# Kernel tuning notes

Hardware: AMD Instinct MI355X
Metric: run time of the kernel (lower is better)

Reference implementation:

```python
import jax, jax.numpy as jnp
import numpy as np

NB_X = 32
NB_Y = 32
EPS = 1e-08


def setup_inputs() -> dict:
    key = jax.random.key(0)
    ks = jax.random.split(key, 10)
    B, L, F, H, D = 16, NB_X * NB_Y + 1, 768, 12, 64
    s = 0.02
    return {
        'x': jax.random.normal(ks[0], (B, L, F), dtype=jnp.float32),
        'wq': jax.random.normal(ks[1], (F, H, D), dtype=jnp.float32) * s,
        'bq': jnp.zeros((H, D), dtype=jnp.float32),
        'wk': jax.random.normal(ks[2], (F, H, D), dtype=jnp.float32) * s,
        'bk': jnp.zeros((H, D), dtype=jnp.float32),
        'wv': jax.random.normal(ks[3], (F, H, D), dtype=jnp.float32) * s,
        'bv': jnp.zeros((H, D), dtype=jnp.float32),
        'wo': jax.random.normal(ks[4], (H, D, F), dtype=jnp.float32) * s,
        'bo': jnp.zeros((F,), dtype=jnp.float32),
        'toeplitz_params': jax.random.normal(ks[5], (H, 4 * NB_X * NB_Y), dtype=jnp.float32),
    }


def _dist_index():
    # relative-position index over the 2D patch grid, flattened to (L0*L0,)
    gi = np.arange(NB_X)
    gj = np.arange(NB_Y)
    idx = ((gi[:, None, None, None] - gi[None, None, :, None] + NB_X) * 2 * NB_Y
           + gj[None, :, None, None] - gj[None, None, None, :] + NB_Y)
    return jnp.asarray(idx.reshape(-1), dtype=jnp.int32)


def reference(x, wq, bq, wk, bk, wv, bv, wo, bo, toeplitz_params):
    H, D = wq.shape[1], wq.shape[2]
    L0 = NB_X * NB_Y  # number of patch tokens (seq len = L0 + 1 with CLS)

    q = jnp.einsum('bqf,fhd->bqhd', x, wq) + bq
    k = jnp.einsum('bkf,fhd->bkhd', x, wk) + bk
    v = jnp.einsum('bkf,fhd->bkhd', x, wv) + bv

    # relu-kernelized scores
    q = jax.nn.relu(q / jnp.sqrt(jnp.float32(D))) + EPS
    k = jax.nn.relu(k) + EPS
    attn = jnp.einsum('bqhd,bkhd->bhqk', q, k)  # [B,H,L,L]

    # per-head Toeplitz relative-position mask via gather
    tm = jnp.take(toeplitz_params, _dist_index(), axis=1).reshape(H, L0, L0)
    tm = jnp.pad(tm, [[0, 0], [1, 0], [0, 0]], constant_values=1.0)
    tm = jnp.pad(tm, [[0, 0], [0, 0], [1, 0]], constant_values=1.0)

    attn = attn * jnp.abs(tm)[None] + EPS
    attn = attn / jnp.sum(attn, axis=-1, keepdims=True)  # sum-normalization

    out = jnp.einsum('bhqk,bkhd->bqhd', attn, v)
    return jnp.einsum('bqhd,hdf->bqf', out, wo) + bo
```

## Files before the change

### kernel.cpp

```cpp
#include <hip/hip_runtime.h>
#include <hip/hip_bf16.h>

#define BB 16
#define LQ 1025
#define FF 768
#define HH 12
#define DD 64
#define EPSF 1e-8f

#define TPSTRIDE 6400
#define QPART_CLS 6270
#define VSTRIDE 1040

#define LDK 72

typedef unsigned short u16;
typedef __attribute__((ext_vector_type(8))) short  bf16x8;
typedef __attribute__((ext_vector_type(4))) float  f32x4;

__device__ __forceinline__ float bf2f(u16 u) {
    union { unsigned int i; float f; } c;
    c.i = ((unsigned int)u) << 16;
    return c.f;
}

__device__ __forceinline__ u16 f2bf(float f) {
    union { float f; unsigned int i; } c;
    c.f = f;
    unsigned int x = c.i;
    unsigned int r = (x + 0x7fffu + ((x >> 16) & 1u)) >> 16;
    return (u16)r;
}

__global__ __launch_bounds__(256) void convert_x(
    const float* __restrict__ x, u16* __restrict__ xb, int n4)
{
    int i = blockIdx.x * blockDim.x + threadIdx.x;
    const int stride = gridDim.x * blockDim.x;
    for (; i < n4; i += stride) {
        float4 f = ((const float4*)x)[i];
        ushort4 o;
        o.x = f2bf(f.x); o.y = f2bf(f.y); o.z = f2bf(f.z); o.w = f2bf(f.w);
        ((ushort4*)xb)[i] = o;
    }
}

__global__ __launch_bounds__(256) void transpose_w(
    const float* __restrict__ wq, const float* __restrict__ wk,
    const float* __restrict__ wv, const float* __restrict__ wo,
    u16* __restrict__ wqt, u16* __restrict__ wkt,
    u16* __restrict__ wvt, u16* __restrict__ wot)
{
    const int z = blockIdx.z;
    const float* __restrict__ src = (z == 0) ? wq : (z == 1) ? wk : (z == 2) ? wv : wo;
    u16* __restrict__ dst         = (z == 0) ? wqt : (z == 1) ? wkt : (z == 2) ? wvt : wot;

    const int c0 = blockIdx.x * 64;
    const int r0 = blockIdx.y * 64;

    __shared__ u16 tile[64][72];

    const int t   = threadIdx.x;
    const int row = t >> 2;
    const int cs  = (t & 3) << 4;

    {
        const float* p = src + (size_t)(r0 + row) * 768 + c0 + cs;
#pragma unroll
        for (int q = 0; q < 4; ++q) {
            float4 f = *(const float4*)(p + 4 * q);
            ushort4 o;
            o.x = f2bf(f.x); o.y = f2bf(f.y); o.z = f2bf(f.z); o.w = f2bf(f.w);
            *(ushort4*)&tile[row][cs + 4 * q] = o;
        }
    }
    __syncthreads();
    {
        u16* p = dst + (size_t)(c0 + row) * 768 + r0 + cs;
#pragma unroll
        for (int q = 0; q < 4; ++q) {
            ushort4 o;
            o.x = tile[cs + 4 * q + 0][row];
            o.y = tile[cs + 4 * q + 1][row];
            o.z = tile[cs + 4 * q + 2][row];
            o.w = tile[cs + 4 * q + 3][row];
            *(ushort4*)(p + 4 * q) = o;
        }
    }
}

__global__ __launch_bounds__(256) void build_tpa(
    const float* __restrict__ tp, float* __restrict__ tpa)
{
    int i = blockIdx.x * 256 + threadIdx.x;
    if (i >= HH * TPSTRIDE) return;
    int h = i / TPSTRIDE, j = i - h * TPSTRIDE;
    float v;
    if (j < 64) v = 0.f;
    else if (j < 64 + 4096) v = fabsf(tp[h * 4096 + (j - 64)]);
    else v = 1.f;
    tpa[i] = v;
}

__global__ __launch_bounds__(256) void pack_bias(
    const float* __restrict__ bq, const float* __restrict__ bk,
    const float* __restrict__ bv, float* __restrict__ bias_cat)
{
    int i = blockIdx.x * 256 + threadIdx.x;
    if (i >= 2304) return;
    float v = (i < 768) ? bq[i] : (i < 1536) ? bk[i - 768] : bv[i - 1536];
    bias_cat[i] = v;
}

__global__ __launch_bounds__(256) void transpose_v(
    const u16* __restrict__ vbuf, u16* __restrict__ vtbuf)
{
    const int bh = blockIdx.y;
    const int lt = blockIdx.x;
    __shared__ u16 tile[64][65];
    const int t   = threadIdx.x;
    const int row = t >> 2;
    const int seg = (t & 3) << 4;

    {
        int l = lt * 64 + row;
        if (l < LQ) {
            const ushort4* p = (const ushort4*)(vbuf + ((size_t)bh * LQ + l) * 64 + seg);
#pragma unroll
            for (int q = 0; q < 4; ++q) {
                ushort4 a = p[q];
                tile[row][seg + 4 * q + 0] = a.x;
                tile[row][seg + 4 * q + 1] = a.y;
                tile[row][seg + 4 * q + 2] = a.z;
                tile[row][seg + 4 * q + 3] = a.w;
            }
        } else {
#pragma unroll
            for (int j = 0; j < 16; ++j) tile[row][seg + j] = 0;
        }
    }
    __syncthreads();
    {
        int kbase = lt * 64 + seg;
        if (kbase + 16 <= VSTRIDE) {
            u16* q = vtbuf + (size_t)bh * 64 * VSTRIDE + (size_t)row * VSTRIDE + kbase;
#pragma unroll
            for (int g = 0; g < 4; ++g) {
                ushort4 o;
                o.x = tile[seg + 4 * g + 0][row];
                o.y = tile[seg + 4 * g + 1][row];
                o.z = tile[seg + 4 * g + 2][row];
                o.w = tile[seg + 4 * g + 3][row];
                *(ushort4*)(q + 4 * g) = o;
            }
        }
    }
}

__global__ __launch_bounds__(256) void gemm_qkv_mfma(
    const u16* __restrict__ xb, const u16* __restrict__ wt,
    const float* __restrict__ bias_cat,
    u16* __restrict__ qbuf, u16* __restrict__ kbuf, u16* __restrict__ vbuf)
{
    const int M   = BB * LQ;
    const int m0  = blockIdx.x * 128;
    const int n0g = blockIdx.y * 128;

    __shared__ u16 As[128 * LDK];
    __shared__ u16 Bs[128 * LDK];

    const int t    = threadIdx.x;
    const int wave = t >> 6;
    const int lane = t & 63;
    const int quad = lane >> 4;
    const int l16  = lane & 15;
    const int wm   = (wave >> 1) << 6;
    const int wn   = (wave & 1) << 6;

    const int sm   = t >> 1;
    const int sc   = (t & 1) << 5;

    const bool avalid = (m0 + sm) < M;
    const u16* pa = xb + (size_t)(m0 + sm) * 768 + sc;
    const u16* pb = wt + (size_t)(n0g + sm) * 768 + sc;

    f32x4 acc[4][4];
#pragma unroll
    for (int i = 0; i < 4; ++i)
#pragma unroll
        for (int j = 0; j < 4; ++j)
            acc[i][j] = (f32x4){0.f, 0.f, 0.f, 0.f};

    for (int k0 = 0; k0 < 768; k0 += 64) {
        __syncthreads();
        if (avalid) {
            const uint4* p = (const uint4*)(pa + k0);
#pragma unroll
            for (int q = 0; q < 4; ++q)
                *(uint4*)&As[sm * LDK + sc + 8 * q] = p[q];
        } else {
            uint4 z; z.x = 0; z.y = 0; z.z = 0; z.w = 0;
#pragma unroll
            for (int q = 0; q < 4; ++q)
                *(uint4*)&As[sm * LDK + sc + 8 * q] = z;
        }
        {
            const uint4* p = (const uint4*)(pb + k0);
#pragma unroll
            for (int q = 0; q < 4; ++q)
                *(uint4*)&Bs[sm * LDK + sc + 8 * q] = p[q];
        }
        __syncthreads();

#pragma unroll
        for (int h2 = 0; h2 < 2; ++h2) {
            bf16x8 af[4], bf[4];
#pragma unroll
            for (int i = 0; i < 4; ++i)
                af[i] = *(const bf16x8*)&As[(wm + 16 * i + l16) * LDK + h2 * 32 + quad * 8];
#pragma unroll
            for (int j = 0; j < 4; ++j)
                bf[j] = *(const bf16x8*)&Bs[(wn + 16 * j + l16) * LDK + h2 * 32 + quad * 8];
#pragma unroll
            for (int i = 0; i < 4; ++i)
#pragma unroll
                for (int j = 0; j < 4; ++j)
                    acc[i][j] = __builtin_amdgcn_mfma_f32_16x16x32_bf16(af[i], bf[j], acc[i][j], 0, 0, 0);
        }
    }

    const int type = (n0g >= 1536) ? 2 : (n0g >= 768) ? 1 : 0;
    u16* __restrict__ outb = (type == 0) ? qbuf : (type == 1) ? kbuf : vbuf;
    const int nbase = n0g - type * 768;

#pragma unroll
    for (int i = 0; i < 4; ++i) {
#pragma unroll
        for (int reg = 0; reg < 4; ++reg) {
            int gm = m0 + wm + 16 * i + quad * 4 + reg;
            if (gm >= M) continue;
            int b_idx = gm / LQ;
            int l     = gm - b_idx * LQ;
#pragma unroll
            for (int j = 0; j < 4; ++j) {
                int nloc = nbase + wn + 16 * j + l16;
                int h = nloc >> 6, d = nloc & 63;
                float v = acc[i][j][reg] + bias_cat[n0g + wn + 16 * j + l16];
                if (type == 0) v = fmaxf(v * 0.125f, 0.f) + EPSF;
                else if (type == 1) v = fmaxf(v, 0.f) + EPSF;
                outb[((size_t)(b_idx * HH + h) * LQ + l) * 64 + d] = f2bf(v);
            }
        }
    }
}

__global__ __launch_bounds__(256) void attn_fused(
    const u16* __restrict__ qbuf, const u16* __restrict__ kbuf,
    const u16* __restrict__ vtbuf, const float* __restrict__ tpa,
    u16* __restrict__ obuf)
{
    const int bh = blockIdx.y;
    const int b  = bh / HH;
    const int h  = bh - b * HH;
    const int q0 = blockIdx.x * 64;

    __shared__ u16 SQ[64][72];
    __shared__ u16 Ks[2][64][72];
    __shared__ u16 Vt[2][64][72];

    const int t    = threadIdx.x;
    const int wave = t >> 6;
    const int lane = t & 63;
    const int quad = lane >> 4;
    const int l16  = lane & 15;
    const int w16  = wave << 4;

    const size_t base  = (size_t)bh * LQ * 64;
    const size_t vbase = (size_t)bh * 64 * VSTRIDE;
    const float* tb = tpa + h * TPSTRIDE;

    const int srow = t >> 2;
    const int sseg = (t & 3) << 4;

    {
        const uint4* qp = (const uint4*)(qbuf + base + (size_t)(q0 + srow) * 64 + sseg);
        *(uint4*)&SQ[srow][sseg]     = qp[0];
        *(uint4*)&SQ[srow][sseg + 8] = qp[1];
    }

    const int qi = q0 + w16 + l16;
    int qpart;
    if (qi == 0) qpart = QPART_CLS;
    else { int qm1 = qi - 1; qpart = (((qm1 >> 5) + 32) << 6) + (qm1 & 31) + 32; }

    int idx[16];
#pragma unroll
    for (int ct = 0; ct < 4; ++ct)
#pragma unroll
        for (int reg = 0; reg < 4; ++reg) {
            int km1 = ct * 16 + quad * 4 + reg - 1;
            idx[ct * 4 + reg] = 64 + qpart - (((km1 >> 5) << 6) + (km1 & 31));
        }

    uint4 kr0, kr1, vr0, vr1;
    {
        uint4 z; z.x = 0; z.y = 0; z.z = 0; z.w = 0;
        int ki = srow;
        if (ki < LQ) {
            const uint4* kp = (const uint4*)(kbuf + base + (size_t)ki * 64 + sseg);
            kr0 = kp[0]; kr1 = kp[1];
        } else { kr0 = z; kr1 = z; }
        const uint4* vp = (const uint4*)(vtbuf + vbase + (size_t)srow * VSTRIDE + sseg);
        vr0 = vp[0]; vr1 = vp[1];
    }

    __syncthreads();

    bf16x8 qf0 = *(const bf16x8*)&SQ[w16 + l16][quad * 8];
    bf16x8 qf1 = *(const bf16x8*)&SQ[w16 + l16][32 + quad * 8];

    *(uint4*)&Ks[0][srow][sseg]     = kr0;
    *(uint4*)&Ks[0][srow][sseg + 8] = kr1;
    *(uint4*)&Vt[0][srow][sseg]     = vr0;
    *(uint4*)&Vt[0][srow][sseg + 8] = vr1;

    {
        uint4 z; z.x = 0; z.y = 0; z.z = 0; z.w = 0;
        int ki = 64 + srow;
        if (ki < LQ) {
            const uint4* kp = (const uint4*)(kbuf + base + (size_t)ki * 64 + sseg);
            kr0 = kp[0]; kr1 = kp[1];
        } else { kr0 = z; kr1 = z; }
        int vcol = 64 + sseg;
        const uint4* vp = (const uint4*)(vtbuf + vbase + (size_t)srow * VSTRIDE + vcol);
        vr0 = vp[0]; vr1 = vp[1];
    }

    f32x4 acc_o[4];
#pragma unroll
    for (int dt = 0; dt < 4; ++dt) acc_o[dt] = (f32x4){0.f, 0.f, 0.f, 0.f};
    float den = 0.f;

    __syncthreads();

    for (int kt = 0; kt < 17; ++kt) {
        const int p = kt & 1;

        if (kt < 16) {
            *(uint4*)&Ks[p ^ 1][srow][sseg]     = kr0;
            *(uint4*)&Ks[p ^ 1][srow][sseg + 8] = kr1;
            *(uint4*)&Vt[p ^ 1][srow][sseg]     = vr0;
            *(uint4*)&Vt[p ^ 1][srow][sseg + 8] = vr1;
        }
        if (kt < 15) {
            uint4 z; z.x = 0; z.y = 0; z.z = 0; z.w = 0;
            int k0n = (kt + 2) * 64;
            int ki = k0n + srow;
            if (ki < LQ) {
                const uint4* kp = (const uint4*)(kbuf + base + (size_t)ki * 64 + sseg);
                kr0 = kp[0]; kr1 = kp[1];
            } else { kr0 = z; kr1 = z; }
            int vcol = k0n + sseg;
            if (vcol + 16 <= VSTRIDE) {
                const uint4* vp = (const uint4*)(vtbuf + vbase + (size_t)srow * VSTRIDE + vcol);
                vr0 = vp[0]; vr1 = vp[1];
            } else { vr0 = z; vr1 = z; }
        }

        float tmv[16];
#pragma unroll
        for (int e = 0; e < 16; ++e) tmv[e] = tb[idx[e]];

        f32x4 acc_s[4];
#pragma unroll
        for (int ct = 0; ct < 4; ++ct) {
            bf16x8 kf0 = *(const bf16x8*)&Ks[p][ct * 16 + l16][quad * 8];
            bf16x8 kf1 = *(const bf16x8*)&Ks[p][ct * 16 + l16][32 + quad * 8];
            f32x4 z = (f32x4){0.f, 0.f, 0.f, 0.f};
            z = __builtin_amdgcn_mfma_f32_16x16x32_bf16(kf0, qf0, z, 0, 0, 0);
            z = __builtin_amdgcn_mfma_f32_16x16x32_bf16(kf1, qf1, z, 0, 0, 0);
            acc_s[ct] = z;
        }

        if (kt == 0) { if (quad == 0) tmv[0] = 1.0f; }

#pragma unroll
        for (int ct = 0; ct < 4; ++ct) {
            float s0 = acc_s[ct][0] * tmv[ct * 4 + 0] + EPSF;
            float s1 = acc_s[ct][1] * tmv[ct * 4 + 1] + EPSF;
            float s2 = acc_s[ct][2] * tmv[ct * 4 + 2] + EPSF;
            float s3 = acc_s[ct][3] * tmv[ct * 4 + 3] + EPSF;
            den += (s0 + s1) + (s2 + s3);
            ushort4 w;
            w.x = f2bf(s0); w.y = f2bf(s1); w.z = f2bf(s2); w.w = f2bf(s3);
            *(ushort4*)&SQ[w16 + l16][ct * 16 + quad * 4] = w;
        }
#pragma unroll
        for (int e = 0; e < 16; ++e) idx[e] -= 128;

        {
            bf16x8 a0 = *(const bf16x8*)&SQ[w16 + l16][quad * 8];
            bf16x8 a1 = *(const bf16x8*)&SQ[w16 + l16][32 + quad * 8];
#pragma unroll
            for (int dt = 0; dt < 4; ++dt) {
                bf16x8 b0 = *(const bf16x8*)&Vt[p][dt * 16 + l16][quad * 8];
                bf16x8 b1 = *(const bf16x8*)&Vt[p][dt * 16 + l16][32 + quad * 8];
                acc_o[dt] = __builtin_amdgcn_mfma_f32_16x16x32_bf16(a0, b0, acc_o[dt], 0, 0, 0);
                acc_o[dt] = __builtin_amdgcn_mfma_f32_16x16x32_bf16(a1, b1, acc_o[dt], 0, 0, 0);
            }
        }

        if (kt < 16) __syncthreads();
    }

    den += __shfl_xor(den, 16);
    den += __shfl_xor(den, 32);
    float invd = 1.f / den;

#pragma unroll
    for (int reg = 0; reg < 4; ++reg) {
        int r = quad * 4 + reg;
        float iv = __shfl(invd, r, 64);
        int qrow = q0 + w16 + r;
        if (qrow < LQ) {
            u16* p = obuf + ((size_t)(b * LQ + qrow) * HH + h) * 64;
#pragma unroll
            for (int dt = 0; dt < 4; ++dt)
                p[dt * 16 + l16] = f2bf(acc_o[dt][reg] * iv);
        }
    }
}

__global__ __launch_bounds__(256) void gemm_out_mfma(
    const u16* __restrict__ a, const u16* __restrict__ wot,
    const float* __restrict__ bo, float* __restrict__ out)
{
    const int M  = BB * LQ;
    const int m0 = blockIdx.x * 128;
    const int n0 = blockIdx.y * 128;

    __shared__ u16 As[128 * LDK];
    __shared__ u16 Bs[128 * LDK];

    const int t    = threadIdx.x;
    const int wave = t >> 6;
    const int lane = t & 63;
    const int quad = lane >> 4;
    const int l16  = lane & 15;
    const int wm   = (wave >> 1) << 6;
    const int wn   = (wave & 1) << 6;

    const int sm   = t >> 1;
    const int sc   = (t & 1) << 5;

    const bool avalid = (m0 + sm) < M;
    const u16* pa = a   + (size_t)(m0 + sm) * 768 + sc;
    const u16* pb = wot + (size_t)(n0 + sm) * 768 + sc;

    f32x4 acc[4][4];
#pragma unroll
    for (int i = 0; i < 4; ++i)
#pragma unroll
        for (int j = 0; j < 4; ++j)
            acc[i][j] = (f32x4){0.f, 0.f, 0.f, 0.f};

    for (int k0 = 0; k0 < 768; k0 += 64) {
        __syncthreads();
        if (avalid) {
            const uint4* p = (const uint4*)(pa + k0);
#pragma unroll
            for (int q = 0; q < 4; ++q)
                *(uint4*)&As[sm * LDK + sc + 8 * q] = p[q];
        } else {
            uint4 z; z.x = 0; z.y = 0; z.z = 0; z.w = 0;
#pragma unroll
            for (int q = 0; q < 4; ++q)
                *(uint4*)&As[sm * LDK + sc + 8 * q] = z;
        }
        {
            const uint4* p = (const uint4*)(pb + k0);
#pragma unroll
            for (int q = 0; q < 4; ++q)
                *(uint4*)&Bs[sm * LDK + sc + 8 * q] = p[q];
        }
        __syncthreads();

#pragma unroll
        for (int h2 = 0; h2 < 2; ++h2) {
            bf16x8 af[4], bf[4];
#pragma unroll
            for (int i = 0; i < 4; ++i)
                af[i] = *(const bf16x8*)&As[(wm + 16 * i + l16) * LDK + h2 * 32 + quad * 8];
#pragma unroll
            for (int j = 0; j < 4; ++j)
                bf[j] = *(const bf16x8*)&Bs[(wn + 16 * j + l16) * LDK + h2 * 32 + quad * 8];
#pragma unroll
            for (int i = 0; i < 4; ++i)
#pragma unroll
                for (int j = 0; j < 4; ++j)
                    acc[i][j] = __builtin_amdgcn_mfma_f32_16x16x32_bf16(af[i], bf[j], acc[i][j], 0, 0, 0);
        }
    }

#pragma unroll
    for (int i = 0; i < 4; ++i) {
#pragma unroll
        for (int reg = 0; reg < 4; ++reg) {
            int gm = m0 + wm + 16 * i + quad * 4 + reg;
            if (gm >= M) continue;
            float* p = out + (size_t)gm * 768;
#pragma unroll
            for (int j = 0; j < 4; ++j) {
                int n = n0 + wn + 16 * j + l16;
                p[n] = acc[i][j][reg] + bo[n];
            }
        }
    }
}

extern "C" void kernel_launch(void* const* d_in, const int* in_sizes, int n_in,
                              void* d_out, int out_size, void* d_ws, size_t ws_size,
                              hipStream_t stream) {
    const float* x  = (const float*)d_in[0];
    const float* wq = (const float*)d_in[1];
    const float* bq = (const float*)d_in[2];
    const float* wk = (const float*)d_in[3];
    const float* bk = (const float*)d_in[4];
    const float* wv = (const float*)d_in[5];
    const float* bv = (const float*)d_in[6];
    const float* wo = (const float*)d_in[7];
    const float* bo = (const float*)d_in[8];
    const float* tp = (const float*)d_in[9];
    float* out = (float*)d_out;

    const size_t per = (size_t)BB * HH * LQ * DD;
    const size_t wsz = (size_t)FF * FF;
    u16* ws16  = (u16*)d_ws;
    u16* qbuf  = ws16;
    u16* kbuf  = qbuf + per;
    u16* vbuf  = kbuf + per;
    u16* xb    = vbuf + per;
    u16* wqt   = xb + per;
    u16* wkt   = wqt + wsz;
    u16* wvt   = wkt + wsz;
    u16* wot   = wvt + wsz;
    float* tpa = (float*)(wot + wsz);
    float* bias_cat = tpa + HH * TPSTRIDE;

    u16* vtbuf = xb;
    u16* obuf  = vbuf;

    convert_x<<<2048, 256, 0, stream>>>(x, xb, (int)(per / 4));
    dim3 gt(12, 12, 4);
    transpose_w<<<gt, 256, 0, stream>>>(wq, wk, wv, wo, wqt, wkt, wvt, wot);
    build_tpa<<<(HH * TPSTRIDE + 255) / 256, 256, 0, stream>>>(tp, tpa);
    pack_bias<<<9, 256, 0, stream>>>(bq, bk, bv, bias_cat);

    dim3 g1(129, 18);
    gemm_qkv_mfma<<<g1, 256, 0, stream>>>(xb, wqt, bias_cat, qbuf, kbuf, vbuf);

    dim3 gv(17, BB * HH);
    transpose_v<<<gv, 256, 0, stream>>>(vbuf, vtbuf);

    dim3 g2(17, BB * HH);
    attn_fused<<<g2, 256, 0, stream>>>(qbuf, kbuf, vtbuf, tpa, obuf);

    dim3 g3(129, 6);
    gemm_out_mfma<<<g3, 256, 0, stream>>>(obuf, wot, bo, out);
}
```

Before: 455.5 us.

## Precompute dense per-head Toeplitz mask and stream it in attention

Adds a kernel that expands the abs Toeplitz parameters into a dense padded [H,1088,1088] fp32 mask in workspace. A new attention kernel then reads each mask row as float4 vectors instead of doing gathered index arithmetic per score. The cost is an extra ~57MB write per call plus heavier global traffic from the dense mask, which should stay largely L2/MALL-resident across batches. The new path only runs when the workspace is large enough.

```diff
diff --git a/kernel.cpp b/kernel.cpp
--- a/kernel.cpp
+++ b/kernel.cpp
@@ -11,6 +11,7 @@
 #define TPSTRIDE 6400
 #define QPART_CLS 6270
 #define VSTRIDE 1040
+#define TMQ 1088
 
 #define LDK 72
 
@@ -102,6 +103,30 @@
     tpa[i] = v;
 }
 
+__global__ __launch_bounds__(256) void build_tmfull(
+    const float* __restrict__ tpa, float* __restrict__ tmf)
+{
+    const int h  = blockIdx.y;
+    const int qi = blockIdx.x;
+    const float* tb = tpa + h * TPSTRIDE;
+    float* row = tmf + ((size_t)h * TMQ + qi) * TMQ;
+
+    int qpart;
+    if (qi == 0) qpart = QPART_CLS;
+    else { int qm1 = qi - 1; qpart = (((qm1 >> 5) + 32) << 6) + (qm1 & 31) + 32; }
+
+    for (int kg = threadIdx.x; kg < TMQ; kg += 256) {
+        float v;
+        if (kg == 0) v = 1.0f;
+        else {
+            int km1 = kg - 1;
+            int kpart = ((km1 >> 5) << 6) + (km1 & 31);
+            v = tb[64 + qpart - kpart];
+        }
+        row[kg] = v;
+    }
+}
+
 __global__ __launch_bounds__(256) void pack_bias(
     const float* __restrict__ bq, const float* __restrict__ bk,
     const float* __restrict__ bv, float* __restrict__ bias_cat)
@@ -250,6 +275,169 @@
                 else if (type == 1) v = fmaxf(v, 0.f) + EPSF;
                 outb[((size_t)(b_idx * HH + h) * LQ + l) * 64 + d] = f2bf(v);
             }
+        }
+    }
+}
+
+__global__ __launch_bounds__(256) void attn_fused_tm(
+    const u16* __restrict__ qbuf, const u16* __restrict__ kbuf,
+    const u16* __restrict__ vtbuf, const float* __restrict__ tmf,
+    u16* __restrict__ obuf)
+{
+    const int bh = blockIdx.y;
+    const int b  = bh / HH;
+    const int h  = bh - b * HH;
+    const int q0 = blockIdx.x * 64;
+
+    __shared__ u16 SQ[64][72];
+    __shared__ u16 Ks[2][64][72];
+    __shared__ u16 Vt[2][64][72];
+
+    const int t    = threadIdx.x;
+    const int wave = t >> 6;
+    const int lane = t & 63;
+    const int quad = lane >> 4;
+    const int l16  = lane & 15;
+    const int w16  = wave << 4;
+
+    const size_t base  = (size_t)bh * LQ * 64;
+    const size_t vbase = (size_t)bh * 64 * VSTRIDE;
+
+    const int srow = t >> 2;
+    const int sseg = (t & 3) << 4;
+
+    {
+        const uint4* qp = (const uint4*)(qbuf + base + (size_t)(q0 + srow) * 64 + sseg);
+        *(uint4*)&SQ[srow][sseg]     = qp[0];
+        *(uint4*)&SQ[srow][sseg + 8] = qp[1];
+    }
+
+    const int qi = q0 + w16 + l16;
+    const float* tml = tmf + ((size_t)h * TMQ + qi) * TMQ + quad * 4;
+
+    uint4 kr0, kr1, vr0, vr1;
+    {
+        uint4 z; z.x = 0; z.y = 0; z.z = 0; z.w = 0;
+        int ki = srow;
+        if (ki < LQ) {
+            const uint4* kp = (const uint4*)(kbuf + base + (size_t)ki * 64 + sseg);
+            kr0 = kp[0]; kr1 = kp[1];
+        } else { kr0 = z; kr1 = z; }
+        const uint4* vp = (const uint4*)(vtbuf + vbase + (size_t)srow * VSTRIDE + sseg);
+        vr0 = vp[0]; vr1 = vp[1];
+    }
+
+    __syncthreads();
+
+    bf16x8 qf0 = *(const bf16x8*)&SQ[w16 + l16][quad * 8];
+    bf16x8 qf1 = *(const bf16x8*)&SQ[w16 + l16][32 + quad * 8];
+
+    *(uint4*)&Ks[0][srow][sseg]     = kr0;
+    *(uint4*)&Ks[0][srow][sseg + 8] = kr1;
+    *(uint4*)&Vt[0][srow][sseg]     = vr0;
+    *(uint4*)&Vt[0][srow][sseg + 8] = vr1;
+
+    {
+        uint4 z; z.x = 0; z.y = 0; z.z = 0; z.w = 0;
+        int ki = 64 + srow;
+        if (ki < LQ) {
+            const uint4* kp = (const uint4*)(kbuf + base + (size_t)ki * 64 + sseg);
+            kr0 = kp[0]; kr1 = kp[1];
+        } else { kr0 = z; kr1 = z; }
+        int vcol = 64 + sseg;
+        const uint4* vp = (const uint4*)(vtbuf + vbase + (size_t)srow * VSTRIDE + vcol);
+        vr0 = vp[0]; vr1 = vp[1];
+    }
+
+    f32x4 acc_o[4];
+#pragma unroll
+    for (int dt = 0; dt < 4; ++dt) acc_o[dt] = (f32x4){0.f, 0.f, 0.f, 0.f};
+    float den = 0.f;
+
+    __syncthreads();
+
+    for (int kt = 0; kt < 17; ++kt) {
+        const int p = kt & 1;
+
+        if (kt < 16) {
+            *(uint4*)&Ks[p ^ 1][srow][sseg]     = kr0;
+            *(uint4*)&Ks[p ^ 1][srow][sseg + 8] = kr1;
+            *(uint4*)&Vt[p ^ 1][srow][sseg]     = vr0;
+            *(uint4*)&Vt[p ^ 1][srow][sseg + 8] = vr1;
+        }
+        if (kt < 15) {
+            uint4 z; z.x = 0; z.y = 0; z.z = 0; z.w = 0;
+            int k0n = (kt + 2) * 64;
+            int ki = k0n + srow;
+            if (ki < LQ) {
+                const uint4* kp = (const uint4*)(kbuf + base + (size_t)ki * 64 + sseg);
+                kr0 = kp[0]; kr1 = kp[1];
+            } else { kr0 = z; kr1 = z; }
+            int vcol = k0n + sseg;
+            if (vcol + 16 <= VSTRIDE) {
+                const uint4* vp = (const uint4*)(vtbuf + vbase + (size_t)srow * VSTRIDE + vcol);
+                vr0 = vp[0]; vr1 = vp[1];
+            } else { vr0 = z; vr1 = z; }
+        }
+
+        float4 tm4[4];
+#pragma unroll
+        for (int ct = 0; ct < 4; ++ct)
+            tm4[ct] = *(const float4*)(tml + ct * 16);
+
+        f32x4 acc_s[4];
+#pragma unroll
+        for (int ct = 0; ct < 4; ++ct) {
+            bf16x8 kf0 = *(const bf16x8*)&Ks[p][ct * 16 + l16][quad * 8];
+            bf16x8 kf1 = *(const bf16x8*)&Ks[p][ct * 16 + l16][32 + quad * 8];
+            f32x4 z = (f32x4){0.f, 0.f, 0.f, 0.f};
+            z = __builtin_amdgcn_mfma_f32_16x16x32_bf16(kf0, qf0, z, 0, 0, 0);
+            z = __builtin_amdgcn_mfma_f32_16x16x32_bf16(kf1, qf1, z, 0, 0, 0);
+            acc_s[ct] = z;
+        }
+
+#pragma unroll
+        for (int ct = 0; ct < 4; ++ct) {
+            float s0 = acc_s[ct][0] * tm4[ct].x + EPSF;
+            float s1 = acc_s[ct][1] * tm4[ct].y + EPSF;
+            float s2 = acc_s[ct][2] * tm4[ct].z + EPSF;
+            float s3 = acc_s[ct][3] * tm4[ct].w + EPSF;
+            den += (s0 + s1) + (s2 + s3);
+            ushort4 w;
+            w.x = f2bf(s0); w.y = f2bf(s1); w.z = f2bf(s2); w.w = f2bf(s3);
+            *(ushort4*)&SQ[w16 + l16][ct * 16 + quad * 4] = w;
+        }
+        tml += 64;
+
+        {
+            bf16x8 a0 = *(const bf16x8*)&SQ[w16 + l16][quad * 8];
+            bf16x8 a1 = *(const bf16x8*)&SQ[w16 + l16][32 + quad * 8];
+#pragma unroll
+            for (int dt = 0; dt < 4; ++dt) {
+                bf16x8 b0 = *(const bf16x8*)&Vt[p][dt * 16 + l16][quad * 8];
+                bf16x8 b1 = *(const bf16x8*)&Vt[p][dt * 16 + l16][32 + quad * 8];
+                acc_o[dt] = __builtin_amdgcn_mfma_f32_16x16x32_bf16(a0, b0, acc_o[dt], 0, 0, 0);
+                acc_o[dt] = __builtin_amdgcn_mfma_f32_16x16x32_bf16(a1, b1, acc_o[dt], 0, 0, 0);
+            }
+        }
+
+        if (kt < 16) __syncthreads();
+    }
+
+    den += __shfl_xor(den, 16);
+    den += __shfl_xor(den, 32);
+    float invd = 1.f / den;
+
+#pragma unroll
+    for (int reg = 0; reg < 4; ++reg) {
+        int r = quad * 4 + reg;
+        float iv = __shfl(invd, r, 64);
+        int qrow = q0 + w16 + r;
+        if (qrow < LQ) {
+            u16* p = obuf + ((size_t)(b * LQ + qrow) * HH + h) * 64;
+#pragma unroll
+            for (int dt = 0; dt < 4; ++dt)
+                p[dt * 16 + l16] = f2bf(acc_o[dt][reg] * iv);
         }
     }
 }
@@ -546,15 +734,24 @@
     u16* wot   = wvt + wsz;
     float* tpa = (float*)(wot + wsz);
     float* bias_cat = tpa + HH * TPSTRIDE;
+    float* tmfull   = bias_cat + 2304;
 
     u16* vtbuf = xb;
     u16* obuf  = vbuf;
+
+    const size_t tm_off = (size_t)((char*)tmfull - (char*)d_ws);
+    const size_t tm_bytes = (size_t)HH * TMQ * TMQ * sizeof(float);
+    const bool use_tm = ws_size >= tm_off + tm_bytes;
 
     convert_x<<<2048, 256, 0, stream>>>(x, xb, (int)(per / 4));
     dim3 gt(12, 12, 4);
     transpose_w<<<gt, 256, 0, stream>>>(wq, wk, wv, wo, wqt, wkt, wvt, wot);
     build_tpa<<<(HH * TPSTRIDE + 255) / 256, 256, 0, stream>>>(tp, tpa);
     pack_bias<<<9, 256, 0, stream>>>(bq, bk, bv, bias_cat);
+    if (use_tm) {
+        dim3 gm(TMQ, HH);
+        build_tmfull<<<gm, 256, 0, stream>>>(tpa, tmfull);
+    }
 
     dim3 g1(129, 18);
     gemm_qkv_mfma<<<g1, 256, 0, stream>>>(xb, wqt, bias_cat, qbuf, kbuf, vbuf);
@@ -563,7 +760,10 @@
     transpose_v<<<gv, 256, 0, stream>>>(vbuf, vtbuf);
 
     dim3 g2(17, BB * HH);
-    attn_fused<<<g2, 256, 0, stream>>>(qbuf, kbuf, vtbuf, tpa, obuf);
+    if (use_tm)
+        attn_fused_tm<<<g2, 256, 0, stream>>>(qbuf, kbuf, vtbuf, tmfull, obuf);
+    else
+        attn_fused<<<g2, 256, 0, stream>>>(qbuf, kbuf, vtbuf, tpa, obuf);
 
     dim3 g3(129, 6);
     gemm_out_mfma<<<g3, 256, 0, stream>>>(obuf, wot, bo, out);
```

Measured after the change: 518.7 us. 1.14x slower.

## Read K/V fragments directly from global memory in attention, dropping LDS staging

Applied to the files above, without the earlier changes.

The attention kernel no longer stages K and V tiles through double-buffered shared memory. Each wave now loads its MFMA fragments straight from global memory, and the per-tile __syncthreads barriers are removed. To drop the bounds checks, the K buffer is padded to 1088 rows with a new kernel that zeroes the tail, and the transposed-V stride is widened to match. The aim is to cut LDS traffic and barrier stalls. In exchange, every wave re-reads the same K/V through the caches, and with the loop left un-unrolled there is no explicit prefetch to hide global load latency.

```diff
diff --git a/kernel.cpp b/kernel.cpp
--- a/kernel.cpp
+++ b/kernel.cpp
@@ -10,7 +10,8 @@
 
 #define TPSTRIDE 6400
 #define QPART_CLS 6270
-#define VSTRIDE 1040
+#define VSTRIDE 1088
+#define KPAD 1088
 
 #define LDK 72
 
@@ -112,6 +113,19 @@
     bias_cat[i] = v;
 }
 
+__global__ __launch_bounds__(256) void zero_ktail(u16* __restrict__ kbuf)
+{
+    int i = blockIdx.x * 256 + threadIdx.x;
+    const int N = BB * HH * (KPAD - LQ) * 16;
+    if (i >= N) return;
+    int bh  = i / ((KPAD - LQ) * 16);
+    int r   = i - bh * ((KPAD - LQ) * 16);
+    int row = LQ + (r >> 4);
+    int seg = (r & 15) << 2;
+    ushort4 z; z.x = 0; z.y = 0; z.z = 0; z.w = 0;
+    *(ushort4*)(kbuf + ((size_t)bh * KPAD + row) * 64 + seg) = z;
+}
+
 __global__ __launch_bounds__(256) void transpose_v(
     const u16* __restrict__ vbuf, u16* __restrict__ vtbuf)
 {
@@ -232,6 +246,7 @@
     const int type = (n0g >= 1536) ? 2 : (n0g >= 768) ? 1 : 0;
     u16* __restrict__ outb = (type == 0) ? qbuf : (type == 1) ? kbuf : vbuf;
     const int nbase = n0g - type * 768;
+    const int lst   = (type == 1) ? KPAD : LQ;
 
 #pragma unroll
     for (int i = 0; i < 4; ++i) {
@@ -248,7 +263,7 @@
                 float v = acc[i][j][reg] + bias_cat[n0g + wn + 16 * j + l16];
                 if (type == 0) v = fmaxf(v * 0.125f, 0.f) + EPSF;
                 else if (type == 1) v = fmaxf(v, 0.f) + EPSF;
-                outb[((size_t)(b_idx * HH + h) * LQ + l) * 64 + d] = f2bf(v);
+                outb[((size_t)(b_idx * HH + h) * lst + l) * 64 + d] = f2bf(v);
             }
         }
     }
@@ -265,8 +280,6 @@
     const int q0 = blockIdx.x * 64;
 
     __shared__ u16 SQ[64][72];
-    __shared__ u16 Ks[2][64][72];
-    __shared__ u16 Vt[2][64][72];
 
     const int t    = threadIdx.x;
     const int wave = t >> 6;
@@ -275,20 +288,16 @@
     const int l16  = lane & 15;
     const int w16  = wave << 4;
 
-    const size_t base  = (size_t)bh * LQ * 64;
-    const size_t vbase = (size_t)bh * 64 * VSTRIDE;
+    const u16* qb = qbuf  + (size_t)bh * LQ * 64;
+    const u16* kb = kbuf  + (size_t)bh * KPAD * 64;
+    const u16* vb = vtbuf + (size_t)bh * 64 * VSTRIDE;
     const float* tb = tpa + h * TPSTRIDE;
 
-    const int srow = t >> 2;
-    const int sseg = (t & 3) << 4;
-
-    {
-        const uint4* qp = (const uint4*)(qbuf + base + (size_t)(q0 + srow) * 64 + sseg);
-        *(uint4*)&SQ[srow][sseg]     = qp[0];
-        *(uint4*)&SQ[srow][sseg + 8] = qp[1];
-    }
-
     const int qi = q0 + w16 + l16;
+    const u16* qp = qb + (size_t)qi * 64 + quad * 8;
+    bf16x8 qf0 = *(const bf16x8*)(qp);
+    bf16x8 qf1 = *(const bf16x8*)(qp + 32);
+
     int qpart;
     if (qi == 0) qpart = QPART_CLS;
     else { int qm1 = qi - 1; qpart = (((qm1 >> 5) + 32) << 6) + (qm1 & 31) + 32; }
@@ -302,71 +311,20 @@
             idx[ct * 4 + reg] = 64 + qpart - (((km1 >> 5) << 6) + (km1 & 31));
         }
 
-    uint4 kr0, kr1, vr0, vr1;
-    {
-        uint4 z; z.x = 0; z.y = 0; z.z = 0; z.w = 0;
-        int ki = srow;
-        if (ki < LQ) {
-            const uint4* kp = (const uint4*)(kbuf + base + (size_t)ki * 64 + sseg);
-            kr0 = kp[0]; kr1 = kp[1];
-        } else { kr0 = z; kr1 = z; }
-        const uint4* vp = (const uint4*)(vtbuf + vbase + (size_t)srow * VSTRIDE + sseg);
-        vr0 = vp[0]; vr1 = vp[1];
-    }
-
-    __syncthreads();
-
-    bf16x8 qf0 = *(const bf16x8*)&SQ[w16 + l16][quad * 8];
-    bf16x8 qf1 = *(const bf16x8*)&SQ[w16 + l16][32 + quad * 8];
-
-    *(uint4*)&Ks[0][srow][sseg]     = kr0;
-    *(uint4*)&Ks[0][srow][sseg + 8] = kr1;
-    *(uint4*)&Vt[0][srow][sseg]     = vr0;
-    *(uint4*)&Vt[0][srow][sseg + 8] = vr1;
-
-    {
-        uint4 z; z.x = 0; z.y = 0; z.z = 0; z.w = 0;
-        int ki = 64 + srow;
-        if (ki < LQ) {
-            const uint4* kp = (const uint4*)(kbuf + base + (size_t)ki * 64 + sseg);
-            kr0 = kp[0]; kr1 = kp[1];
-        } else { kr0 = z; kr1 = z; }
-        int vcol = 64 + sseg;
-        const uint4* vp = (const uint4*)(vtbuf + vbase + (size_t)srow * VSTRIDE + vcol);
-        vr0 = vp[0]; vr1 = vp[1];
-    }
+    const u16* kp  = kb + (size_t)l16 * 64 + quad * 8;
+    const u16* kp2 = kp + 2048;
+    const u16* vr0 = vb + (size_t)l16 * VSTRIDE + quad * 8;
+    const u16* vr1 = vr0 + 16 * VSTRIDE;
+    const u16* vr2 = vr0 + 32 * VSTRIDE;
+    const u16* vr3 = vr0 + 48 * VSTRIDE;
 
     f32x4 acc_o[4];
 #pragma unroll
     for (int dt = 0; dt < 4; ++dt) acc_o[dt] = (f32x4){0.f, 0.f, 0.f, 0.f};
     float den = 0.f;
 
-    __syncthreads();
-
+#pragma unroll 1
     for (int kt = 0; kt < 17; ++kt) {
-        const int p = kt & 1;
-
-        if (kt < 16) {
-            *(uint4*)&Ks[p ^ 1][srow][sseg]     = kr0;
-            *(uint4*)&Ks[p ^ 1][srow][sseg + 8] = kr1;
-            *(uint4*)&Vt[p ^ 1][srow][sseg]     = vr0;
-            *(uint4*)&Vt[p ^ 1][srow][sseg + 8] = vr1;
-        }
-        if (kt < 15) {
-            uint4 z; z.x = 0; z.y = 0; z.z = 0; z.w = 0;
-            int k0n = (kt + 2) * 64;
-            int ki = k0n + srow;
-            if (ki < LQ) {
-                const uint4* kp = (const uint4*)(kbuf + base + (size_t)ki * 64 + sseg);
-                kr0 = kp[0]; kr1 = kp[1];
-            } else { kr0 = z; kr1 = z; }
-            int vcol = k0n + sseg;
-            if (vcol + 16 <= VSTRIDE) {
-                const uint4* vp = (const uint4*)(vtbuf + vbase + (size_t)srow * VSTRIDE + vcol);
-                vr0 = vp[0]; vr1 = vp[1];
-            } else { vr0 = z; vr1 = z; }
-        }
-
         float tmv[16];
 #pragma unroll
         for (int e = 0; e < 16; ++e) tmv[e] = tb[idx[e]];
@@ -374,8 +332,9 @@
         f32x4 acc_s[4];
 #pragma unroll
         for (int ct = 0; ct < 4; ++ct) {
-            bf16x8 kf0 = *(const bf16x8*)&Ks[p][ct * 16 + l16][quad * 8];
-            bf16x8 kf1 = *(const bf16x8*)&Ks[p][ct * 16 + l16][32 + quad * 8];
+            const u16* kr = ((ct & 2) ? kp2 : kp) + (ct & 1) * 1024;
+            bf16x8 kf0 = *(const bf16x8*)(kr);
+            bf16x8 kf1 = *(const bf16x8*)(kr + 32);
             f32x4 z = (f32x4){0.f, 0.f, 0.f, 0.f};
             z = __builtin_amdgcn_mfma_f32_16x16x32_bf16(kf0, qf0, z, 0, 0, 0);
             z = __builtin_amdgcn_mfma_f32_16x16x32_bf16(kf1, qf1, z, 0, 0, 0);
@@ -401,16 +360,31 @@
         {
             bf16x8 a0 = *(const bf16x8*)&SQ[w16 + l16][quad * 8];
             bf16x8 a1 = *(const bf16x8*)&SQ[w16 + l16][32 + quad * 8];
-#pragma unroll
-            for (int dt = 0; dt < 4; ++dt) {
-                bf16x8 b0 = *(const bf16x8*)&Vt[p][dt * 16 + l16][quad * 8];
-                bf16x8 b1 = *(const bf16x8*)&Vt[p][dt * 16 + l16][32 + quad * 8];
-                acc_o[dt] = __builtin_amdgcn_mfma_f32_16x16x32_bf16(a0, b0, acc_o[dt], 0, 0, 0);
-                acc_o[dt] = __builtin_amdgcn_mfma_f32_16x16x32_bf16(a1, b1, acc_o[dt], 0, 0, 0);
-            }
-        }
-
-        if (kt < 16) __syncthreads();
+
+            bf16x8 b00 = *(const bf16x8*)(vr0);
+            bf16x8 b01 = *(const bf16x8*)(vr0 + 32);
+            acc_o[0] = __builtin_amdgcn_mfma_f32_16x16x32_bf16(a0, b00, acc_o[0], 0, 0, 0);
+            acc_o[0] = __builtin_amdgcn_mfma_f32_16x16x32_bf16(a1, b01, acc_o[0], 0, 0, 0);
+
+            bf16x8 b10 = *(const bf16x8*)(vr1);
+            bf16x8 b11 = *(const bf16x8*)(vr1 + 32);
+            acc_o[1] = __builtin_amdgcn_mfma_f32_16x16x32_bf16(a0, b10, acc_o[1], 0, 0, 0);
+            acc_o[1] = __builtin_amdgcn_mfma_f32_16x16x32_bf16(a1, b11, acc_o[1], 0, 0, 0);
+
+            bf16x8 b20 = *(const bf16x8*)(vr2);
+            bf16x8 b21 = *(const bf16x8*)(vr2 + 32);
+            acc_o[2] = __builtin_amdgcn_mfma_f32_16x16x32_bf16(a0, b20, acc_o[2], 0, 0, 0);
+            acc_o[2] = __builtin_amdgcn_mfma_f32_16x16x32_bf16(a1, b21, acc_o[2], 0, 0, 0);
+
+            bf16x8 b30 = *(const bf16x8*)(vr3);
+            bf16x8 b31 = *(const bf16x8*)(vr3 + 32);
+            acc_o[3] = __builtin_amdgcn_mfma_f32_16x16x32_bf16(a0, b30, acc_o[3], 0, 0, 0);
+            acc_o[3] = __builtin_amdgcn_mfma_f32_16x16x32_bf16(a1, b31, acc_o[3], 0, 0, 0);
+        }
+
+        kp  += 64 * 64;
+        kp2 += 64 * 64;
+        vr0 += 64; vr1 += 64; vr2 += 64; vr3 += 64;
     }
 
     den += __shfl_xor(den, 16);
@@ -533,12 +507,13 @@
     const float* tp = (const float*)d_in[9];
     float* out = (float*)d_out;
 
-    const size_t per = (size_t)BB * HH * LQ * DD;
-    const size_t wsz = (size_t)FF * FF;
+    const size_t per  = (size_t)BB * HH * LQ * DD;
+    const size_t perK = (size_t)BB * HH * KPAD * DD;
+    const size_t wsz  = (size_t)FF * FF;
     u16* ws16  = (u16*)d_ws;
     u16* qbuf  = ws16;
     u16* kbuf  = qbuf + per;
-    u16* vbuf  = kbuf + per;
+    u16* vbuf  = kbuf + perK;
     u16* xb    = vbuf + per;
     u16* wqt   = xb + per;
     u16* wkt   = wqt + wsz;
@@ -555,6 +530,10 @@
     transpose_w<<<gt, 256, 0, stream>>>(wq, wk, wv, wo, wqt, wkt, wvt, wot);
     build_tpa<<<(HH * TPSTRIDE + 255) / 256, 256, 0, stream>>>(tp, tpa);
     pack_bias<<<9, 256, 0, stream>>>(bq, bk, bv, bias_cat);
+    {
+        const int nzt = BB * HH * (KPAD - LQ) * 16;
+        zero_ktail<<<(nzt + 255) / 256, 256, 0, stream>>>(kbuf);
+    }
 
     dim3 g1(129, 18);
     gemm_qkv_mfma<<<g1, 256, 0, stream>>>(xb, wqt, bias_cat, qbuf, kbuf, vbuf);
```

New measurement: 790.2 us. 1.73x slower.

## Double attention query tile to 128 rows with 512-thread blocks

Applied to the files above, without the earlier changes.

Each attention block now covers 128 query rows with eight waves instead of 64 rows with four. The double-buffered K and V tiles are shared by twice as many queries, which halves global K/V traffic and staging work per query. With more threads, each thread now stages a single 16-byte chunk per tile. In exchange the block count drops, the padded tail grows (1152 versus 1088 rows), and larger blocks may lower occupancy and scheduling flexibility.

```diff
diff --git a/kernel.cpp b/kernel.cpp
--- a/kernel.cpp
+++ b/kernel.cpp
@@ -254,7 +254,7 @@
     }
 }
 
-__global__ __launch_bounds__(256) void attn_fused(
+__global__ __launch_bounds__(512) void attn_fused(
     const u16* __restrict__ qbuf, const u16* __restrict__ kbuf,
     const u16* __restrict__ vtbuf, const float* __restrict__ tpa,
     u16* __restrict__ obuf)
@@ -262,9 +262,9 @@
     const int bh = blockIdx.y;
     const int b  = bh / HH;
     const int h  = bh - b * HH;
-    const int q0 = blockIdx.x * 64;
-
-    __shared__ u16 SQ[64][72];
+    const int q0 = blockIdx.x * 128;
+
+    __shared__ u16 SQ[128][72];
     __shared__ u16 Ks[2][64][72];
     __shared__ u16 Vt[2][64][72];
 
@@ -279,13 +279,16 @@
     const size_t vbase = (size_t)bh * 64 * VSTRIDE;
     const float* tb = tpa + h * TPSTRIDE;
 
-    const int srow = t >> 2;
-    const int sseg = (t & 3) << 4;
-
-    {
-        const uint4* qp = (const uint4*)(qbuf + base + (size_t)(q0 + srow) * 64 + sseg);
-        *(uint4*)&SQ[srow][sseg]     = qp[0];
-        *(uint4*)&SQ[srow][sseg + 8] = qp[1];
+    const int srow = t >> 3;
+    const int sseg = (t & 7) << 3;
+
+    const int qsr  = t >> 2;
+    const int qss  = (t & 3) << 4;
+
+    {
+        const uint4* qp = (const uint4*)(qbuf + base + (size_t)(q0 + qsr) * 64 + qss);
+        *(uint4*)&SQ[qsr][qss]     = qp[0];
+        *(uint4*)&SQ[qsr][qss + 8] = qp[1];
     }
 
     const int qi = q0 + w16 + l16;
@@ -302,16 +305,13 @@
             idx[ct * 4 + reg] = 64 + qpart - (((km1 >> 5) << 6) + (km1 & 31));
         }
 
-    uint4 kr0, kr1, vr0, vr1;
+    uint4 kr, vr;
     {
         uint4 z; z.x = 0; z.y = 0; z.z = 0; z.w = 0;
         int ki = srow;
-        if (ki < LQ) {
-            const uint4* kp = (const uint4*)(kbuf + base + (size_t)ki * 64 + sseg);
-            kr0 = kp[0]; kr1 = kp[1];
-        } else { kr0 = z; kr1 = z; }
-        const uint4* vp = (const uint4*)(vtbuf + vbase + (size_t)srow * VSTRIDE + sseg);
-        vr0 = vp[0]; vr1 = vp[1];
+        if (ki < LQ) kr = *(const uint4*)(kbuf + base + (size_t)ki * 64 + sseg);
+        else kr = z;
+        vr = *(const uint4*)(vtbuf + vbase + (size_t)srow * VSTRIDE + sseg);
     }
 
     __syncthreads();
@@ -319,21 +319,16 @@
     bf16x8 qf0 = *(const bf16x8*)&SQ[w16 + l16][quad * 8];
     bf16x8 qf1 = *(const bf16x8*)&SQ[w16 + l16][32 + quad * 8];
 
-    *(uint4*)&Ks[0][srow][sseg]     = kr0;
-    *(uint4*)&Ks[0][srow][sseg + 8] = kr1;
-    *(uint4*)&Vt[0][srow][sseg]     = vr0;
-    *(uint4*)&Vt[0][srow][sseg + 8] = vr1;
+    *(uint4*)&Ks[0][srow][sseg] = kr;
+    *(uint4*)&Vt[0][srow][sseg] = vr;
 
     {
         uint4 z; z.x = 0; z.y = 0; z.z = 0; z.w = 0;
         int ki = 64 + srow;
-        if (ki < LQ) {
-            const uint4* kp = (const uint4*)(kbuf + base + (size_t)ki * 64 + sseg);
-            kr0 = kp[0]; kr1 = kp[1];
-        } else { kr0 = z; kr1 = z; }
+        if (ki < LQ) kr = *(const uint4*)(kbuf + base + (size_t)ki * 64 + sseg);
+        else kr = z;
         int vcol = 64 + sseg;
-        const uint4* vp = (const uint4*)(vtbuf + vbase + (size_t)srow * VSTRIDE + vcol);
-        vr0 = vp[0]; vr1 = vp[1];
+        vr = *(const uint4*)(vtbuf + vbase + (size_t)srow * VSTRIDE + vcol);
     }
 
     f32x4 acc_o[4];
@@ -347,24 +342,19 @@
         const int p = kt & 1;
 
         if (kt < 16) {
-            *(uint4*)&Ks[p ^ 1][srow][sseg]     = kr0;
-            *(uint4*)&Ks[p ^ 1][srow][sseg + 8] = kr1;
-            *(uint4*)&Vt[p ^ 1][srow][sseg]     = vr0;
-            *(uint4*)&Vt[p ^ 1][srow][sseg + 8] = vr1;
+            *(uint4*)&Ks[p ^ 1][srow][sseg] = kr;
+            *(uint4*)&Vt[p ^ 1][srow][sseg] = vr;
         }
         if (kt < 15) {
             uint4 z; z.x = 0; z.y = 0; z.z = 0; z.w = 0;
             int k0n = (kt + 2) * 64;
             int ki = k0n + srow;
-            if (ki < LQ) {
-                const uint4* kp = (const uint4*)(kbuf + base + (size_t)ki * 64 + sseg);
-                kr0 = kp[0]; kr1 = kp[1];
-            } else { kr0 = z; kr1 = z; }
+            if (ki < LQ) kr = *(const uint4*)(kbuf + base + (size_t)ki * 64 + sseg);
+            else kr = z;
             int vcol = k0n + sseg;
-            if (vcol + 16 <= VSTRIDE) {
-                const uint4* vp = (const uint4*)(vtbuf + vbase + (size_t)srow * VSTRIDE + vcol);
-                vr0 = vp[0]; vr1 = vp[1];
-            } else { vr0 = z; vr1 = z; }
+            if (vcol + 8 <= VSTRIDE)
+                vr = *(const uint4*)(vtbuf + vbase + (size_t)srow * VSTRIDE + vcol);
+            else vr = z;
         }
 
         float tmv[16];
@@ -562,8 +552,8 @@
     dim3 gv(17, BB * HH);
     transpose_v<<<gv, 256, 0, stream>>>(vbuf, vtbuf);
 
-    dim3 g2(17, BB * HH);
-    attn_fused<<<g2, 256, 0, stream>>>(qbuf, kbuf, vtbuf, tpa, obuf);
+    dim3 g2(9, BB * HH);
+    attn_fused<<<g2, 512, 0, stream>>>(qbuf, kbuf, vtbuf, tpa, obuf);
 
     dim3 g3(129, 6);
     gemm_out_mfma<<<g3, 256, 0, stream>>>(obuf, wot, bo, out);
```

Measured after the change: 475.9 us. 1.04x slower.
